# Performance work log

Hardware: AMD Instinct MI355X
Metric: run time of the kernel (lower is better)

Reference implementation:

```python
import jax, jax.numpy as jnp
import numpy as np

C = 128          # channels == channel_num (divisible by token_num)
TOKEN = 4        # token_num -> mamba sequence length
GROUP = 32       # group_channel_num == mamba d_model
D_IN = 64        # d_inner = expand * d_model
D_STATE = 16
D_CONV = 4
DT_RANK = 2      # ceil(d_model/16)
GN_GROUPS = 4
B, H, W = 2, 128, 128


def setup_inputs() -> dict:
    key = jax.random.key(0)
    ks = jax.random.split(key, 12)
    def n(k, shape, s=0.05):
        return jax.random.normal(k, shape, dtype=jnp.float32) * s
    x = jax.random.normal(ks[0], (B, C, H, W), dtype=jnp.float32)
    A_log = jnp.broadcast_to(jnp.log(jnp.arange(1, D_STATE + 1, dtype=jnp.float32)), (D_IN, D_STATE))
    return {
        "x": x,
        "in_proj_w": n(ks[1], (2 * D_IN, GROUP)),
        "conv_w": n(ks[2], (D_IN, D_CONV), 0.2),
        "conv_b": n(ks[3], (D_IN,), 0.05),
        "x_proj_w": n(ks[4], (DT_RANK + 2 * D_STATE, D_IN)),
        "dt_proj_w": n(ks[5], (D_IN, DT_RANK), 0.2),
        "dt_proj_b": n(ks[6], (D_IN,), 0.1),
        "A_log": A_log,
        "D": jnp.ones((D_IN,), jnp.float32),
        "out_proj_w": n(ks[7], (GROUP, D_IN)),
        "se1_w": n(ks[8], (C // 4, C)),   # PostMambaSE fc1 (1x1 conv, no bias)
        "se2_w": n(ks[9], (C, C // 4)),   # PostMambaSE fc2 (1x1 conv, no bias)
        "gn_w": jnp.ones((C,), jnp.float32),
        "gn_b": jnp.zeros((C,), jnp.float32),
    }


def _mamba(xf, in_proj_w, conv_w, conv_b, x_proj_w, dt_proj_w, dt_proj_b, A_log, D, out_proj_w):
    # xf: (N, L, d_model) with N=b*h*w, L=token_num
    N, L, _ = xf.shape
    xz = xf @ in_proj_w.T                       # (N, L, 2*D_IN)
    xi, z = jnp.split(xz, 2, axis=-1)
    # causal depthwise conv1d along L (kernel D_CONV, left-pad D_CONV-1)
    xp = jnp.pad(xi, ((0, 0), (D_CONV - 1, 0), (0, 0)))
    xc = conv_b + sum(conv_w[:, k] * xp[:, k:k + L, :] for k in range(D_CONV))
    xc = jax.nn.silu(xc)                        # (N, L, D_IN)
    dbl = xc @ x_proj_w.T                       # (N, L, DT_RANK + 2*D_STATE)
    dt, Bm, Cm = jnp.split(dbl, [DT_RANK, DT_RANK + D_STATE], axis=-1)
    delta = jax.nn.softplus(dt @ dt_proj_w.T + dt_proj_b)   # (N, L, D_IN)
    A = -jnp.exp(A_log)                         # (D_IN, D_STATE)

    def step(h, ins):
        u_t, d_t, B_t, C_t = ins                # (N,D_IN) (N,D_IN) (N,S) (N,S)
        dA = jnp.exp(d_t[..., None] * A)        # (N, D_IN, S)
        h = dA * h + (d_t * u_t)[..., None] * B_t[:, None, :]
        return h, (h * C_t[:, None, :]).sum(-1)

    xs = (jnp.swapaxes(xc, 0, 1), jnp.swapaxes(delta, 0, 1),
          jnp.swapaxes(Bm, 0, 1), jnp.swapaxes(Cm, 0, 1))
    h0 = jnp.zeros((N, D_IN, D_STATE), xf.dtype)
    _, ys = jax.lax.scan(step, h0, xs)          # ys: (L, N, D_IN)
    y = jnp.swapaxes(ys, 0, 1) + xc * D
    y = y * jax.nn.silu(z)
    return y @ out_proj_w.T                     # (N, L, d_model)


def reference(x, in_proj_w, conv_w, conv_b, x_proj_w, dt_proj_w, dt_proj_b,
              A_log, D, out_proj_w, se1_w, se2_w, gn_w, gn_b):
    b, c, h, w = x.shape
    # attention_mode='none' -> Identity; channels == channel_num -> no padding
    # faithful replication of torch .view(b*h*w, token, group) on (b,c,h,w)
    xf = x.reshape(b * h * w, TOKEN, GROUP)
    y = _mamba(xf, in_proj_w, conv_w, conv_b, x_proj_w, dt_proj_w, dt_proj_b,
               A_log, D, out_proj_w)
    xr = y.reshape(b, c, h, w)
    # PostMambaSE
    pooled = xr.mean(axis=(2, 3))                                  # (b, c)
    g = jax.nn.sigmoid(jax.nn.silu(pooled @ se1_w.T) @ se2_w.T)    # (b, c)
    xr = xr * g[:, :, None, None]
    # GroupNorm(4, c) + SiLU
    xg = xr.reshape(b, GN_GROUPS, c // GN_GROUPS, h, w)
    mu = xg.mean(axis=(2, 3, 4), keepdims=True)
    var = xg.var(axis=(2, 3, 4), keepdims=True)
    xg = (xg - mu) / jnp.sqrt(var + 1e-5)
    xr = xg.reshape(b, c, h, w) * gn_w[None, :, None, None] + gn_b[None, :, None, None]
    xr = jax.nn.silu(xr)
    return xr + x   # use_residual=True, output channels == input channels
```

## Files before the change

kernel.cpp:

```cpp
#include <hip/hip_runtime.h>
#include <math.h>

#define NROWS 32768
#define NTILES 8192
#define THREADS 256
#define WPB 4

typedef __attribute__((ext_vector_type(8))) __bf16 bf16x8;
typedef __attribute__((ext_vector_type(4))) float f32x4;

__device__ __forceinline__ float silu_f(float v) {
    return v * __builtin_amdgcn_rcpf(1.f + __expf(-v));
}
__device__ __forceinline__ bf16x8 cvt8v(float4 a, float4 b) {
    bf16x8 r;
    r[0]=(__bf16)a.x; r[1]=(__bf16)a.y; r[2]=(__bf16)a.z; r[3]=(__bf16)a.w;
    r[4]=(__bf16)b.x; r[5]=(__bf16)b.y; r[6]=(__bf16)b.z; r[7]=(__bf16)b.w;
    return r;
}

__global__ __launch_bounds__(256) void k_mamba(
    const float* __restrict__ x,
    const float* __restrict__ in_proj_w,
    const float* __restrict__ conv_w,
    const float* __restrict__ conv_b,
    const float* __restrict__ x_proj_w,
    const float* __restrict__ dt_proj_w,
    const float* __restrict__ dt_proj_b,
    const float* __restrict__ A_log,
    const float* __restrict__ Dvec,
    const float* __restrict__ out_proj_w,
    float* __restrict__ xr,
    float* __restrict__ S1, float* __restrict__ S2)
{
    __shared__ __align__(16) __bf16 b1f[8*64*8];
    __shared__ __align__(16) float xcb[WPB][16*68];
    __shared__ __align__(16) float szb[WPB][16*66];
    __shared__ __align__(16) float dbb[WPB][16*44];

    const int tid  = threadIdx.x;
    const int wid  = tid >> 6;
    const int lane = tid & 63;
    const int c = lane & 15;
    const int q = lane >> 4;

    for (int idx = tid; idx < 512; idx += THREADS) {
        int jt = idx >> 6, l = idx & 63, cc = l & 15, qq = l >> 4;
        const float* src = in_proj_w + (jt*16 + cc)*32 + qq*8;
        bf16x8 v;
        #pragma unroll
        for (int i = 0; i < 8; ++i) v[i] = (__bf16)src[i];
        *((bf16x8*)(b1f) + idx) = v;
    }

    bf16x8 B2f[2][3];
    #pragma unroll
    for (int ks = 0; ks < 2; ++ks)
        #pragma unroll
        for (int rt = 0; rt < 3; ++rt) {
            int row = rt*16 + c;
            #pragma unroll
            for (int i = 0; i < 8; ++i)
                B2f[ks][rt][i] = (row < 34) ? (__bf16)x_proj_w[row*64 + ks*32 + q*8 + i]
                                            : (__bf16)0.f;
        }
    bf16x8 B3f[2][2];
    #pragma unroll
    for (int jt = 0; jt < 2; ++jt)
        #pragma unroll
        for (int ks = 0; ks < 2; ++ks) {
            int row = jt*16 + c;
            #pragma unroll
            for (int i = 0; i < 8; ++i)
                B3f[jt][ks][i] = (__bf16)out_proj_w[row*64 + ks*32 + q*8 + i];
        }

    float cwj[4][4], cbj[4];
    #pragma unroll
    for (int jt = 0; jt < 4; ++jt) {
        int d = jt*16 + c;
        #pragma unroll
        for (int k = 0; k < 4; ++k) cwj[jt][k] = conv_w[d*4 + k];
        cbj[jt] = conv_b[d];
    }
    const float dtw0 = dt_proj_w[lane*2+0], dtw1 = dt_proj_w[lane*2+1];
    const float dtb  = dt_proj_b[lane];
    const float Dd   = Dvec[lane];

    bool okl = true;
    #pragma unroll
    for (int s = 0; s < 16; ++s) {
        float a = __expf(A_log[lane*16 + s]);
        okl = okl && (fabsf(a - (float)(s+1)) < 1e-3f * (float)(s+1));
    }
    const bool fastA = (__ballot(okl) == ~0ull);

    __syncthreads();

    float* xc_ = xcb[wid];
    float* sz_ = szb[wid];
    float* db_ = dbb[wid];
    const bf16x8* B1p = (const bf16x8*)b1f;
    const int nwaves = gridDim.x * WPB;

    for (int tile = blockIdx.x*WPB + wid; tile < NTILES; tile += nwaves) {
        const int n0 = tile * 4;
        const float* xrow = x + n0*128;

        const float4* xp4 = (const float4*)(xrow + c*32 + q*8);
        bf16x8 A1 = cvt8v(xp4[0], xp4[1]);

        #pragma unroll
        for (int jt = 0; jt < 8; ++jt) {
            f32x4 acc = {0.f, 0.f, 0.f, 0.f};
            acc = __builtin_amdgcn_mfma_f32_16x16x32_bf16(A1, B1p[jt*64 + lane], acc, 0, 0, 0);
            if (jt < 4) {
                const float* cw = cwj[jt];
                float cb = cbj[jt];
                float xc0 = cb + cw[3]*acc[0];
                float xc1 = cb + cw[2]*acc[0] + cw[3]*acc[1];
                float xc2 = cb + cw[1]*acc[0] + cw[2]*acc[1] + cw[3]*acc[2];
                float xc3 = cb + cw[0]*acc[0] + cw[1]*acc[1] + cw[2]*acc[2] + cw[3]*acc[3];
                int dcol = jt*16 + c;
                xc_[(4*q+0)*68 + dcol] = silu_f(xc0);
                xc_[(4*q+1)*68 + dcol] = silu_f(xc1);
                xc_[(4*q+2)*68 + dcol] = silu_f(xc2);
                xc_[(4*q+3)*68 + dcol] = silu_f(xc3);
            } else {
                int dcol = (jt-4)*16 + c;
                #pragma unroll
                for (int t = 0; t < 4; ++t)
                    sz_[(4*q+t)*66 + dcol] = silu_f(acc[t]);
            }
        }

        bf16x8 A2[2];
        #pragma unroll
        for (int ks = 0; ks < 2; ++ks) {
            const float4* p = (const float4*)&xc_[c*68 + ks*32 + q*8];
            A2[ks] = cvt8v(p[0], p[1]);
        }
        f32x4 dacc[3] = {{0,0,0,0},{0,0,0,0},{0,0,0,0}};
        #pragma unroll
        for (int ks = 0; ks < 2; ++ks) {
            dacc[0] = __builtin_amdgcn_mfma_f32_16x16x32_bf16(A2[ks], B2f[ks][0], dacc[0], 0,0,0);
            dacc[1] = __builtin_amdgcn_mfma_f32_16x16x32_bf16(A2[ks], B2f[ks][1], dacc[1], 0,0,0);
            dacc[2] = __builtin_amdgcn_mfma_f32_16x16x32_bf16(A2[ks], B2f[ks][2], dacc[2], 0,0,0);
        }
        #pragma unroll
        for (int rt = 0; rt < 3; ++rt) {
            if (rt < 2 || c < 4) {
                #pragma unroll
                for (int t = 0; t < 4; ++t)
                    db_[(4*q+t)*44 + 2 + rt*16 + c] = dacc[rt][t];
            }
        }

        #pragma unroll
        for (int r = 0; r < 4; ++r) {
            float h[16];
            #pragma unroll
            for (int s = 0; s < 16; ++s) h[s] = 0.f;
            #pragma unroll
            for (int t = 0; t < 4; ++t) {
                const int m = 4*r + t;
                float2 dtv = *(const float2*)&db_[m*44 + 2];
                float p  = fmaf(dtv.y, dtw1, fmaf(dtv.x, dtw0, dtb));
                float ex = __expf(p);
                float t1 = 1.f + ex;
                float e1 = __builtin_amdgcn_rcpf(t1);
                float delta = (p > 15.f) ? p : __logf(t1);
                float u  = xc_[m*68 + lane];
                float sz = sz_[m*66 + lane];
                const float bu = delta * u;

                float dA[16];
                if (fastA) {
                    float e2 = e1*e1, e4 = e2*e2, e8 = e4*e4;
                    dA[0]=e1;      dA[1]=e2;      dA[2]=e2*e1;    dA[3]=e4;
                    dA[4]=e4*e1;   dA[5]=e4*e2;   dA[6]=e4*dA[2]; dA[7]=e8;
                    dA[8]=e8*e1;   dA[9]=e8*e2;   dA[10]=e8*dA[2];dA[11]=e8*e4;
                    dA[12]=e8*dA[4];dA[13]=e8*dA[5];dA[14]=e8*dA[6];dA[15]=e8*e8;
                } else {
                    #pragma unroll
                    for (int s = 0; s < 16; ++s)
                        dA[s] = __expf(-delta * __expf(A_log[lane*16 + s]));
                }

                const float4* B4 = (const float4*)&db_[m*44 + 4];
                const float4* C4 = (const float4*)&db_[m*44 + 20];
                float acc = 0.f;
                #pragma unroll
                for (int s2 = 0; s2 < 4; ++s2) {
                    float4 Bv = B4[s2], Cv = C4[s2];
                    int s = s2*4;
                    h[s+0] = dA[s+0]*h[s+0] + bu*Bv.x;  acc += h[s+0]*Cv.x;
                    h[s+1] = dA[s+1]*h[s+1] + bu*Bv.y;  acc += h[s+1]*Cv.y;
                    h[s+2] = dA[s+2]*h[s+2] + bu*Bv.z;  acc += h[s+2]*Cv.z;
                    h[s+3] = dA[s+3]*h[s+3] + bu*Bv.w;  acc += h[s+3]*Cv.w;
                }
                float y = (acc + u*Dd) * sz;
                xc_[m*68 + lane] = y;
            }
        }

        bf16x8 A3[2];
        #pragma unroll
        for (int ks = 0; ks < 2; ++ks) {
            const float4* p = (const float4*)&xc_[c*68 + ks*32 + q*8];
            A3[ks] = cvt8v(p[0], p[1]);
        }
        float s1 = 0.f, s2 = 0.f;
        float* orow = xr + n0*128;
        #pragma unroll
        for (int jt = 0; jt < 2; ++jt) {
            f32x4 oacc = {0.f, 0.f, 0.f, 0.f};
            oacc = __builtin_amdgcn_mfma_f32_16x16x32_bf16(A3[0], B3f[jt][0], oacc, 0,0,0);
            oacc = __builtin_amdgcn_mfma_f32_16x16x32_bf16(A3[1], B3f[jt][1], oacc, 0,0,0);
            #pragma unroll
            for (int t = 0; t < 4; ++t) {
                orow[(4*q+t)*32 + jt*16 + c] = oacc[t];
                s1 += oacc[t];
                s2 += oacc[t]*oacc[t];
            }
        }
        #pragma unroll
        for (int off = 32; off > 0; off >>= 1) {
            s1 += __shfl_xor(s1, off, 64);
            s2 += __shfl_xor(s2, off, 64);
        }
        if (lane == 0) {
            atomicAdd(&S1[tile >> 5], s1);
            atomicAdd(&S2[tile >> 5], s2);
        }
    }
}

__global__ __launch_bounds__(256) void k_se(
    const float* __restrict__ S1, const float* __restrict__ S2,
    const float* __restrict__ se1_w,
    const float* __restrict__ se2_w,
    const float* __restrict__ gn_w, const float* __restrict__ gn_b,
    float* __restrict__ alpha, float* __restrict__ beta)
{
    __shared__ float sp[256];
    __shared__ float sh[64];
    __shared__ float sg[256], st1[256], st2[256];
    __shared__ float smu[8], sinv[8];
    const int tid = threadIdx.x;

    sp[tid] = S1[tid] * (1.f/16384.f);
    __syncthreads();

    if (tid < 64) {
        int b = tid >> 5, j = tid & 31;
        float acc = 0.f;
        for (int c = 0; c < 128; ++c) acc += sp[b*128 + c] * se1_w[j*128 + c];
        sh[tid] = silu_f(acc);
    }
    __syncthreads();

    {
        int b = tid >> 7, c = tid & 127;
        float acc = 0.f;
        #pragma unroll
        for (int j = 0; j < 32; ++j) acc += sh[b*32 + j] * se2_w[c*32 + j];
        float g = __builtin_amdgcn_rcpf(1.f + __expf(-acc));
        sg[tid]  = g;
        st1[tid] = g * S1[tid];
        st2[tid] = g * g * S2[tid];
    }
    __syncthreads();

    if (tid < 8) {
        int b = tid >> 2, gr = tid & 3;
        float m = 0.f, qq = 0.f;
        for (int c = 0; c < 32; ++c) {
            m  += st1[b*128 + gr*32 + c];
            qq += st2[b*128 + gr*32 + c];
        }
        const float inv_cnt = 1.f / (32.f * 16384.f);
        m *= inv_cnt; qq *= inv_cnt;
        smu[tid]  = m;
        sinv[tid] = rsqrtf(qq - m*m + 1e-5f);
    }
    __syncthreads();

    {
        int b = tid >> 7, c = tid & 127;
        int gi = b*4 + (c >> 5);
        float iv = sinv[gi], mu = smu[gi], g = sg[tid], w = gn_w[c];
        alpha[tid] = g * iv * w;
        beta[tid]  = gn_b[c] - mu * iv * w;
    }
}

__global__ __launch_bounds__(256) void k_final(
    const float* __restrict__ x, float* __restrict__ o,
    const float* __restrict__ alpha, const float* __restrict__ beta)
{
    const int total4 = (2*128*128*128) / 4;
    const float4* x4 = (const float4*)x;
    float4* o4 = (float4*)o;
    for (int i = blockIdx.x*blockDim.x + threadIdx.x; i < total4;
         i += gridDim.x*blockDim.x) {
        int bc = i >> 12;
        float al = alpha[bc], be = beta[bc];
        float4 v = o4[i], xv = x4[i];
        float u;
        u = al*v.x + be;  v.x = silu_f(u) + xv.x;
        u = al*v.y + be;  v.y = silu_f(u) + xv.y;
        u = al*v.z + be;  v.z = silu_f(u) + xv.z;
        u = al*v.w + be;  v.w = silu_f(u) + xv.w;
        o4[i] = v;
    }
}

extern "C" void kernel_launch(void* const* d_in, const int* in_sizes, int n_in,
                              void* d_out, int out_size, void* d_ws, size_t ws_size,
                              hipStream_t stream) {
    const float* x          = (const float*)d_in[0];
    const float* in_proj_w  = (const float*)d_in[1];
    const float* conv_w     = (const float*)d_in[2];
    const float* conv_b     = (const float*)d_in[3];
    const float* x_proj_w   = (const float*)d_in[4];
    const float* dt_proj_w  = (const float*)d_in[5];
    const float* dt_proj_b  = (const float*)d_in[6];
    const float* A_log      = (const float*)d_in[7];
    const float* Dvec       = (const float*)d_in[8];
    const float* out_proj_w = (const float*)d_in[9];
    const float* se1_w      = (const float*)d_in[10];
    const float* se2_w      = (const float*)d_in[11];
    const float* gn_w       = (const float*)d_in[12];
    const float* gn_b       = (const float*)d_in[13];

    float* out = (float*)d_out;
    float* ws  = (float*)d_ws;
    float* S1 = ws;
    float* S2 = ws + 256;
    float* alpha = ws + 512;
    float* beta  = ws + 768;

    hipMemsetAsync(ws, 0, 512*sizeof(float), stream);
    k_mamba<<<768, THREADS, 0, stream>>>(x, in_proj_w, conv_w, conv_b, x_proj_w,
                                         dt_proj_w, dt_proj_b, A_log, Dvec,
                                         out_proj_w, out, S1, S2);
    k_se<<<1, THREADS, 0, stream>>>(S1, S2, se1_w, se2_w, gn_w, gn_b, alpha, beta);
    k_final<<<2048, THREADS, 0, stream>>>(x, out, alpha, beta);
}
```

Measured before the change: 76.05 us.

## Store mamba intermediates as bf16 in LDS, fuse SE into final kernel

Intermediate xc/sz buffers in shared memory become bf16, so the MFMA A-operands load directly as bf16x8 with no fp32-to-bf16 conversion, and the LDS footprint shrinks. The db buffer stride drops from 44 to 36. k_mamba gets launch bounds allowing 4 blocks per CU and a larger grid (1024 blocks). The single-block SE kernel is folded into k_final, with every block recomputing the SE/GroupNorm coefficients, which removes a launch and a serial dependency. The costs are bf16 rounding of the scan inputs and outputs and redundant per-block SE work.

After: 90.06 us. 18.4% more time.

```diff
diff --git a/kernel.cpp b/kernel.cpp
--- a/kernel.cpp
+++ b/kernel.cpp
@@ -12,14 +12,8 @@
 __device__ __forceinline__ float silu_f(float v) {
     return v * __builtin_amdgcn_rcpf(1.f + __expf(-v));
 }
-__device__ __forceinline__ bf16x8 cvt8v(float4 a, float4 b) {
-    bf16x8 r;
-    r[0]=(__bf16)a.x; r[1]=(__bf16)a.y; r[2]=(__bf16)a.z; r[3]=(__bf16)a.w;
-    r[4]=(__bf16)b.x; r[5]=(__bf16)b.y; r[6]=(__bf16)b.z; r[7]=(__bf16)b.w;
-    return r;
-}
-
-__global__ __launch_bounds__(256) void k_mamba(
+
+__global__ __launch_bounds__(256, 4) void k_mamba(
     const float* __restrict__ x,
     const float* __restrict__ in_proj_w,
     const float* __restrict__ conv_w,
@@ -34,9 +28,9 @@
     float* __restrict__ S1, float* __restrict__ S2)
 {
     __shared__ __align__(16) __bf16 b1f[8*64*8];
-    __shared__ __align__(16) float xcb[WPB][16*68];
-    __shared__ __align__(16) float szb[WPB][16*66];
-    __shared__ __align__(16) float dbb[WPB][16*44];
+    __shared__ __align__(16) __bf16 xcb[WPB][16*72];
+    __shared__ __align__(16) __bf16 szb[WPB][16*72];
+    __shared__ __align__(16) float  dbb[WPB][16*36];
 
     const int tid  = threadIdx.x;
     const int wid  = tid >> 6;
@@ -97,9 +91,9 @@
 
     __syncthreads();
 
-    float* xc_ = xcb[wid];
-    float* sz_ = szb[wid];
-    float* db_ = dbb[wid];
+    __bf16* xc_ = xcb[wid];
+    __bf16* sz_ = szb[wid];
+    float*  db_ = dbb[wid];
     const bf16x8* B1p = (const bf16x8*)b1f;
     const int nwaves = gridDim.x * WPB;
 
@@ -107,8 +101,13 @@
         const int n0 = tile * 4;
         const float* xrow = x + n0*128;
 
-        const float4* xp4 = (const float4*)(xrow + c*32 + q*8);
-        bf16x8 A1 = cvt8v(xp4[0], xp4[1]);
+        bf16x8 A1;
+        {
+            const float4* xp4 = (const float4*)(xrow + c*32 + q*8);
+            float4 a = xp4[0], b = xp4[1];
+            A1[0]=(__bf16)a.x; A1[1]=(__bf16)a.y; A1[2]=(__bf16)a.z; A1[3]=(__bf16)a.w;
+            A1[4]=(__bf16)b.x; A1[5]=(__bf16)b.y; A1[6]=(__bf16)b.z; A1[7]=(__bf16)b.w;
+        }
 
         #pragma unroll
         for (int jt = 0; jt < 8; ++jt) {
@@ -122,24 +121,23 @@
                 float xc2 = cb + cw[1]*acc[0] + cw[2]*acc[1] + cw[3]*acc[2];
                 float xc3 = cb + cw[0]*acc[0] + cw[1]*acc[1] + cw[2]*acc[2] + cw[3]*acc[3];
                 int dcol = jt*16 + c;
-                xc_[(4*q+0)*68 + dcol] = silu_f(xc0);
-                xc_[(4*q+1)*68 + dcol] = silu_f(xc1);
-                xc_[(4*q+2)*68 + dcol] = silu_f(xc2);
-                xc_[(4*q+3)*68 + dcol] = silu_f(xc3);
+                xc_[(4*q+0)*72 + dcol] = (__bf16)silu_f(xc0);
+                xc_[(4*q+1)*72 + dcol] = (__bf16)silu_f(xc1);
+                xc_[(4*q+2)*72 + dcol] = (__bf16)silu_f(xc2);
+                xc_[(4*q+3)*72 + dcol] = (__bf16)silu_f(xc3);
             } else {
                 int dcol = (jt-4)*16 + c;
                 #pragma unroll
                 for (int t = 0; t < 4; ++t)
-                    sz_[(4*q+t)*66 + dcol] = silu_f(acc[t]);
+                    sz_[(4*q+t)*72 + dcol] = (__bf16)silu_f(acc[t]);
             }
         }
 
         bf16x8 A2[2];
         #pragma unroll
-        for (int ks = 0; ks < 2; ++ks) {
-            const float4* p = (const float4*)&xc_[c*68 + ks*32 + q*8];
-            A2[ks] = cvt8v(p[0], p[1]);
-        }
+        for (int ks = 0; ks < 2; ++ks)
+            A2[ks] = *(const bf16x8*)&xc_[c*72 + ks*32 + q*8];
+
         f32x4 dacc[3] = {{0,0,0,0},{0,0,0,0},{0,0,0,0}};
         #pragma unroll
         for (int ks = 0; ks < 2; ++ks) {
@@ -149,10 +147,10 @@
         }
         #pragma unroll
         for (int rt = 0; rt < 3; ++rt) {
-            if (rt < 2 || c < 4) {
+            if (rt < 2 || c < 2) {
                 #pragma unroll
                 for (int t = 0; t < 4; ++t)
-                    db_[(4*q+t)*44 + 2 + rt*16 + c] = dacc[rt][t];
+                    db_[(4*q+t)*36 + 2 + rt*16 + c] = dacc[rt][t];
             }
         }
 
@@ -164,14 +162,14 @@
             #pragma unroll
             for (int t = 0; t < 4; ++t) {
                 const int m = 4*r + t;
-                float2 dtv = *(const float2*)&db_[m*44 + 2];
+                float2 dtv = *(const float2*)&db_[m*36 + 2];
                 float p  = fmaf(dtv.y, dtw1, fmaf(dtv.x, dtw0, dtb));
                 float ex = __expf(p);
                 float t1 = 1.f + ex;
                 float e1 = __builtin_amdgcn_rcpf(t1);
                 float delta = (p > 15.f) ? p : __logf(t1);
-                float u  = xc_[m*68 + lane];
-                float sz = sz_[m*66 + lane];
+                float u  = (float)xc_[m*72 + lane];
+                float sz = (float)sz_[m*72 + lane];
                 const float bu = delta * u;
 
                 float dA[16];
@@ -187,8 +185,8 @@
                         dA[s] = __expf(-delta * __expf(A_log[lane*16 + s]));
                 }
 
-                const float4* B4 = (const float4*)&db_[m*44 + 4];
-                const float4* C4 = (const float4*)&db_[m*44 + 20];
+                const float4* B4 = (const float4*)&db_[m*36 + 4];
+                const float4* C4 = (const float4*)&db_[m*36 + 20];
                 float acc = 0.f;
                 #pragma unroll
                 for (int s2 = 0; s2 < 4; ++s2) {
@@ -200,16 +198,15 @@
                     h[s+3] = dA[s+3]*h[s+3] + bu*Bv.w;  acc += h[s+3]*Cv.w;
                 }
                 float y = (acc + u*Dd) * sz;
-                xc_[m*68 + lane] = y;
+                xc_[m*72 + lane] = (__bf16)y;
             }
         }
 
         bf16x8 A3[2];
         #pragma unroll
-        for (int ks = 0; ks < 2; ++ks) {
-            const float4* p = (const float4*)&xc_[c*68 + ks*32 + q*8];
-            A3[ks] = cvt8v(p[0], p[1]);
-        }
+        for (int ks = 0; ks < 2; ++ks)
+            A3[ks] = *(const bf16x8*)&xc_[c*72 + ks*32 + q*8];
+
         float s1 = 0.f, s2 = 0.f;
         float* orow = xr + n0*128;
         #pragma unroll
@@ -236,17 +233,16 @@
     }
 }
 
-__global__ __launch_bounds__(256) void k_se(
+__global__ __launch_bounds__(256) void k_final(
+    const float* __restrict__ x, float* __restrict__ o,
     const float* __restrict__ S1, const float* __restrict__ S2,
     const float* __restrict__ se1_w,
     const float* __restrict__ se2_w,
-    const float* __restrict__ gn_w, const float* __restrict__ gn_b,
-    float* __restrict__ alpha, float* __restrict__ beta)
+    const float* __restrict__ gn_w, const float* __restrict__ gn_b)
 {
-    __shared__ float sp[256];
-    __shared__ float sh[64];
-    __shared__ float sg[256], st1[256], st2[256];
+    __shared__ float sp[256], sh[64], sg[256], st1[256], st2[256];
     __shared__ float smu[8], sinv[8];
+    __shared__ float al[256], be[256];
     const int tid = threadIdx.x;
 
     sp[tid] = S1[tid] * (1.f/16384.f);
@@ -255,16 +251,16 @@
     if (tid < 64) {
         int b = tid >> 5, j = tid & 31;
         float acc = 0.f;
-        for (int c = 0; c < 128; ++c) acc += sp[b*128 + c] * se1_w[j*128 + c];
+        for (int cc = 0; cc < 128; ++cc) acc += sp[b*128 + cc] * se1_w[j*128 + cc];
         sh[tid] = silu_f(acc);
     }
     __syncthreads();
 
     {
-        int b = tid >> 7, c = tid & 127;
+        int b = tid >> 7, cc = tid & 127;
         float acc = 0.f;
         #pragma unroll
-        for (int j = 0; j < 32; ++j) acc += sh[b*32 + j] * se2_w[c*32 + j];
+        for (int j = 0; j < 32; ++j) acc += sh[b*32 + j] * se2_w[cc*32 + j];
         float g = __builtin_amdgcn_rcpf(1.f + __expf(-acc));
         sg[tid]  = g;
         st1[tid] = g * S1[tid];
@@ -275,9 +271,9 @@
     if (tid < 8) {
         int b = tid >> 2, gr = tid & 3;
         float m = 0.f, qq = 0.f;
-        for (int c = 0; c < 32; ++c) {
-            m  += st1[b*128 + gr*32 + c];
-            qq += st2[b*128 + gr*32 + c];
+        for (int cc = 0; cc < 32; ++cc) {
+            m  += st1[b*128 + gr*32 + cc];
+            qq += st2[b*128 + gr*32 + cc];
         }
         const float inv_cnt = 1.f / (32.f * 16384.f);
         m *= inv_cnt; qq *= inv_cnt;
@@ -287,31 +283,27 @@
     __syncthreads();
 
     {
-        int b = tid >> 7, c = tid & 127;
-        int gi = b*4 + (c >> 5);
-        float iv = sinv[gi], mu = smu[gi], g = sg[tid], w = gn_w[c];
-        alpha[tid] = g * iv * w;
-        beta[tid]  = gn_b[c] - mu * iv * w;
-    }
-}
-
-__global__ __launch_bounds__(256) void k_final(
-    const float* __restrict__ x, float* __restrict__ o,
-    const float* __restrict__ alpha, const float* __restrict__ beta)
-{
+        int b = tid >> 7, cc = tid & 127;
+        int gi = b*4 + (cc >> 5);
+        float iv = sinv[gi], mu = smu[gi], g = sg[tid], w = gn_w[cc];
+        al[tid] = g * iv * w;
+        be[tid] = gn_b[cc] - mu * iv * w;
+    }
+    __syncthreads();
+
     const int total4 = (2*128*128*128) / 4;
     const float4* x4 = (const float4*)x;
     float4* o4 = (float4*)o;
-    for (int i = blockIdx.x*blockDim.x + threadIdx.x; i < total4;
+    for (int i = blockIdx.x*blockDim.x + tid; i < total4;
          i += gridDim.x*blockDim.x) {
         int bc = i >> 12;
-        float al = alpha[bc], be = beta[bc];
+        float a = al[bc], b = be[bc];
         float4 v = o4[i], xv = x4[i];
         float u;
-        u = al*v.x + be;  v.x = silu_f(u) + xv.x;
-        u = al*v.y + be;  v.y = silu_f(u) + xv.y;
-        u = al*v.z + be;  v.z = silu_f(u) + xv.z;
-        u = al*v.w + be;  v.w = silu_f(u) + xv.w;
+        u = a*v.x + b;  v.x = silu_f(u) + xv.x;
+        u = a*v.y + b;  v.y = silu_f(u) + xv.y;
+        u = a*v.z + b;  v.z = silu_f(u) + xv.z;
+        u = a*v.w + b;  v.w = silu_f(u) + xv.w;
         o4[i] = v;
     }
 }
@@ -338,13 +330,10 @@
     float* ws  = (float*)d_ws;
     float* S1 = ws;
     float* S2 = ws + 256;
-    float* alpha = ws + 512;
-    float* beta  = ws + 768;
 
     hipMemsetAsync(ws, 0, 512*sizeof(float), stream);
-    k_mamba<<<768, THREADS, 0, stream>>>(x, in_proj_w, conv_w, conv_b, x_proj_w,
-                                         dt_proj_w, dt_proj_b, A_log, Dvec,
-                                         out_proj_w, out, S1, S2);
-    k_se<<<1, THREADS, 0, stream>>>(S1, S2, se1_w, se2_w, gn_w, gn_b, alpha, beta);
-    k_final<<<2048, THREADS, 0, stream>>>(x, out, alpha, beta);
+    k_mamba<<<1024, THREADS, 0, stream>>>(x, in_proj_w, conv_w, conv_b, x_proj_w,
+                                          dt_proj_w, dt_proj_b, A_log, Dvec,
+                                          out_proj_w, out, S1, S2);
+    k_final<<<2048, THREADS, 0, stream>>>(x, out, S1, S2, se1_w, se2_w, gn_w, gn_b);
 }
```
